# Kernel optimization log

Measured on AMD Instinct MI355X. Metric: run time of the kernel, lower is better.

Reference implementation:

```python
import jax, jax.numpy as jnp
import numpy as np

B, T, C = 8, 1024, 1024
EPS = 1e-5
NEG_INF = -1e38


def layernorm(x, w, b):
    mu = jnp.mean(x, axis=-1, keepdims=True)
    var = jnp.var(x, axis=-1, keepdims=True)
    return (x - mu) * jax.lax.rsqrt(var + EPS) * w + b


def wkv_scan(w, u, k, v):
    """Numerically-stable RWKV-4 WKV recurrence (forward direction).
    w: [C] (negative decay), u: [C] bonus, k, v: [B, T, C]. Returns [B, T, C]."""
    kt = jnp.swapaxes(k, 0, 1)  # [T, B, C]
    vt = jnp.swapaxes(v, 0, 1)
    bsz = k.shape[0]
    a0 = jnp.zeros((bsz, C), k.dtype)
    b0 = jnp.zeros((bsz, C), k.dtype)
    p0 = jnp.full((bsz, C), NEG_INF, k.dtype)

    def step(carry, inp):
        a, b, p = carry
        kk, vv = inp
        # output at current step (with bonus u on current token)
        q = jnp.maximum(p, u + kk)
        e1 = jnp.exp(p - q)
        e2 = jnp.exp(u + kk - q)
        out = (e1 * a + e2 * vv) / (e1 * b + e2)
        # decay state and absorb current token
        q2 = jnp.maximum(p + w, kk)
        f1 = jnp.exp(p + w - q2)
        f2 = jnp.exp(kk - q2)
        return (f1 * a + f2 * vv, f1 * b + f2, q2), out

    _, outs = jax.lax.scan(step, (a0, b0, p0), (kt, vt))
    return jnp.swapaxes(outs, 0, 1)  # [B, T, C]


def setup_inputs() -> dict:
    key = jax.random.key(0)
    ks = jax.random.split(key, 12)
    s = 0.02
    d = {}
    d["x"] = jax.random.normal(ks[0], (B, T, C), jnp.float32)
    d["ln1_w"] = jnp.ones((C,), jnp.float32)
    d["ln1_b"] = jnp.zeros((C,), jnp.float32)
    d["ln2_w"] = jnp.ones((C,), jnp.float32)
    d["ln2_b"] = jnp.zeros((C,), jnp.float32)
    d["Wr"] = jax.random.normal(ks[1], (C, C), jnp.float32) * s
    d["Wk"] = jax.random.normal(ks[2], (C, C), jnp.float32) * s
    d["Wv"] = jax.random.normal(ks[3], (C, C), jnp.float32) * s
    d["Wo"] = jax.random.normal(ks[4], (C, C), jnp.float32) * s
    d["decay"] = jax.random.normal(ks[5], (C,), jnp.float32) * 0.1
    d["u"] = jax.random.normal(ks[6], (C,), jnp.float32) * 0.1
    d["Wfk"] = jax.random.normal(ks[7], (4 * C, C), jnp.float32) * s
    d["Wfv"] = jax.random.normal(ks[8], (C, 4 * C), jnp.float32) * s
    d["Wfr"] = jax.random.normal(ks[9], (C, C), jnp.float32) * s
    return d


def reference(x, ln1_w, ln1_b, ln2_w, ln2_b, Wr, Wk, Wv, Wo, decay, u, Wfk, Wfv, Wfr):
    # --- bidirectional time-mix (WKV attention) ---
    xn = layernorm(x, ln1_w, ln1_b)
    r = jax.nn.sigmoid(xn @ Wr.T)
    k = xn @ Wk.T
    v = xn @ Wv.T
    w = -jnp.exp(decay)  # per-channel negative decay
    wkv_f = wkv_scan(w, u, k, v)
    wkv_b = jnp.flip(wkv_scan(w, u, jnp.flip(k, axis=1), jnp.flip(v, axis=1)), axis=1)
    wkv = 0.5 * (wkv_f + wkv_b)
    x = x + (r * wkv) @ Wo.T
    # --- channel-mix FFN ---
    xn2 = layernorm(x, ln2_w, ln2_b)
    kk = jnp.square(jax.nn.relu(xn2 @ Wfk.T))  # [B, T, 4C]
    x = x + jax.nn.sigmoid(xn2 @ Wfr.T) * (kk @ Wfv.T)
    return x
```

## Files before the change

kernel.cpp:

```cpp
#include <hip/hip_runtime.h>
#include <cstdint>
#include <cstddef>

typedef unsigned short u16;
typedef __bf16 bf16_t;
typedef bf16_t bf16x8 __attribute__((ext_vector_type(8)));
typedef float f32x4 __attribute__((ext_vector_type(4)));

#define GCH 16
#define TCH 64

static __device__ __forceinline__ float bf2f(u16 v) {
    union { unsigned int u; float f; } cv;
    cv.u = ((unsigned int)v) << 16;
    return cv.f;
}
static __device__ __forceinline__ u16 f2bf(float f) {
    union { float f; unsigned int u; } cv;
    cv.f = f;
    unsigned int r = 0x7fffu + ((cv.u >> 16) & 1u);
    return (u16)((cv.u + r) >> 16);
}

struct F2BFSegs { const float* src[7]; u16* dst[7]; int n4[7]; };

__global__ __launch_bounds__(256)
void f2bf_all(F2BFSegs s)
{
    const int seg = blockIdx.y;
    const int i = blockIdx.x * 256 + threadIdx.x;
    if (i < s.n4[seg]) {
        float4 f = ((const float4*)s.src[seg])[i];
        ushort4 o;
        o.x = f2bf(f.x); o.y = f2bf(f.y); o.z = f2bf(f.z); o.w = f2bf(f.w);
        ((ushort4*)s.dst[seg])[i] = o;
    }
}

template<int BF16IN>
__global__ __launch_bounds__(256)
void ln_kernel(const void* __restrict__ xin, const float* __restrict__ w,
               const float* __restrict__ b, u16* __restrict__ out)
{
    const int row = blockIdx.x;
    const int tid = threadIdx.x;
    float vals[4];
    if (BF16IN) {
        const ushort4 uv = ((const ushort4*)((const u16*)xin + (size_t)row * 1024))[tid];
        vals[0] = bf2f(uv.x); vals[1] = bf2f(uv.y);
        vals[2] = bf2f(uv.z); vals[3] = bf2f(uv.w);
    } else {
        const float4 f = ((const float4*)((const float*)xin + (size_t)row * 1024))[tid];
        vals[0] = f.x; vals[1] = f.y; vals[2] = f.z; vals[3] = f.w;
    }
    float s  = vals[0] + vals[1] + vals[2] + vals[3];
    float ss = vals[0]*vals[0] + vals[1]*vals[1] + vals[2]*vals[2] + vals[3]*vals[3];
    for (int off = 32; off; off >>= 1) {
        s  += __shfl_down(s, off, 64);
        ss += __shfl_down(ss, off, 64);
    }
    __shared__ float redS[4], redQ[4];
    if ((tid & 63) == 0) { redS[tid >> 6] = s; redQ[tid >> 6] = ss; }
    __syncthreads();
    s  = redS[0] + redS[1] + redS[2] + redS[3];
    ss = redQ[0] + redQ[1] + redQ[2] + redQ[3];
    const float mu  = s * (1.f / 1024.f);
    const float var = ss * (1.f / 1024.f) - mu * mu;
    const float rs  = rsqrtf(var + 1e-5f);
    const float4 wv = ((const float4*)w)[tid];
    const float4 bv = ((const float4*)b)[tid];
    ushort4 o;
    o.x = f2bf((vals[0] - mu) * rs * wv.x + bv.x);
    o.y = f2bf((vals[1] - mu) * rs * wv.y + bv.y);
    o.z = f2bf((vals[2] - mu) * rs * wv.z + bv.z);
    o.w = f2bf((vals[3] - mu) * rs * wv.w + bv.w);
    ((ushort4*)(out + (size_t)row * 1024))[tid] = o;
}

template<int EPI>
__global__ __launch_bounds__(256)
void gemm_bt(const u16* __restrict__ A, const u16* __restrict__ B,
             int M, int N, int K,
             void* __restrict__ outp,
             const void* __restrict__ aux1, const void* __restrict__ aux2)
{
    __shared__ u16 lA[128 * 64];
    __shared__ u16 lB[128 * 64];
    const int tid  = threadIdx.x;
    const int wave = tid >> 6;
    const int lane = tid & 63;
    const int q    = lane >> 4;
    const int l16  = lane & 15;
    const long mBase = (long)blockIdx.x * 128;
    const long nBase = (long)blockIdx.y * 128;
    const int wm = (wave >> 1) * 64;
    const int wn = (wave & 1) * 64;

    f32x4 acc[4][4];
#pragma unroll
    for (int i = 0; i < 4; ++i)
#pragma unroll
        for (int j = 0; j < 4; ++j)
#pragma unroll
            for (int r = 0; r < 4; ++r) acc[i][j][r] = 0.f;

    const int srow = tid >> 3;
    const int scol = ((tid & 7) ^ (srow & 7)) * 8;
    const int ldsW = wave * 512;
    const int swz = l16 & 7;

    for (int kb = 0; kb < K; kb += 64) {
        __syncthreads();
#pragma unroll
        for (int c = 0; c < 4; ++c) {
            const int row = c * 32 + srow;
            const u16* ga = A + (mBase + row) * (long)K + kb + scol;
            const u16* gb = B + (nBase + row) * (long)K + kb + scol;
            __builtin_amdgcn_global_load_lds(
                (const __attribute__((address_space(1))) void*)ga,
                (__attribute__((address_space(3))) void*)(lA + c * 2048 + ldsW),
                16, 0, 0);
            __builtin_amdgcn_global_load_lds(
                (const __attribute__((address_space(1))) void*)gb,
                (__attribute__((address_space(3))) void*)(lB + c * 2048 + ldsW),
                16, 0, 0);
        }
        __syncthreads();
#pragma unroll
        for (int ks = 0; ks < 2; ++ks) {
            const int grp = ((ks * 4 + q) ^ swz) * 8;
            bf16x8 af[4], bfm[4];
#pragma unroll
            for (int i = 0; i < 4; ++i) {
                af[i]  = *(const bf16x8*)(lA + (wm + i * 16 + l16) * 64 + grp);
                bfm[i] = *(const bf16x8*)(lB + (wn + i * 16 + l16) * 64 + grp);
            }
#pragma unroll
            for (int i = 0; i < 4; ++i)
#pragma unroll
                for (int j = 0; j < 4; ++j)
                    acc[i][j] = __builtin_amdgcn_mfma_f32_16x16x32_bf16(
                        af[i], bfm[j], acc[i][j], 0, 0, 0);
        }
    }

    if (EPI == 5 || EPI == 6) {
        u16* optr; long sN, cb;
        if (EPI == 5) {
            const long seg = nBase >> 10;
            optr = (u16*)(seg == 0 ? outp
                        : seg == 1 ? (void*)aux1 : (void*)aux2);
            sN = 1024; cb = (nBase & 1023) + wn + l16;
        } else {
            if (nBase < 4096) { optr = (u16*)outp; sN = 4096; cb = nBase + wn + l16; }
            else { optr = (u16*)aux1; sN = 1024; cb = (nBase - 4096) + wn + l16; }
        }
#pragma unroll
        for (int i = 0; i < 4; ++i)
#pragma unroll
            for (int r = 0; r < 4; ++r) {
                const long row = mBase + wm + i * 16 + q * 4 + r;
                const long rowOff = row * sN + cb;
#pragma unroll
                for (int j = 0; j < 4; ++j) {
                    const float val = acc[i][j][r];
                    float t;
                    if (EPI == 5) t = val;
                    else if (nBase < 4096) t = val > 0.f ? val * val : 0.f;
                    else t = __fdividef(1.f, 1.f + __expf(-val));
                    optr[rowOff + j * 16] = f2bf(t);
                }
            }
    } else {
        const long colBase = nBase + wn + l16;
#pragma unroll
        for (int i = 0; i < 4; ++i) {
#pragma unroll
            for (int r = 0; r < 4; ++r) {
                const long row = mBase + wm + i * 16 + q * 4 + r;
                const long rowOff = row * (long)N;
#pragma unroll
                for (int j = 0; j < 4; ++j) {
                    const long idx = rowOff + colBase + j * 16;
                    const float val = acc[i][j][r];
                    if (EPI == 1) {
                        ((u16*)outp)[idx] = f2bf(((const float*)aux1)[idx] + val);
                    } else {
                        const float t = bf2f(((const u16*)aux1)[idx])
                                      + bf2f(((const u16*)aux2)[idx]) * val;
                        ((float*)outp)[idx] = t;
                    }
                }
            }
        }
    }
}

__global__ __launch_bounds__(64)
void wkv_sum(const u16* __restrict__ kbuf, const u16* __restrict__ vbuf,
             const float* __restrict__ decay,
             float* __restrict__ sumA, float* __restrict__ sumB,
             float* __restrict__ sumP)
{
    const int c   = blockIdx.x * 64 + threadIdx.x;
    const int bt  = blockIdx.y;
    const int dir = blockIdx.z & 1;
    const int g   = blockIdx.z >> 1;
    const long base = (long)bt * (1024 * 1024) + c;
    const long stride = dir ? -1024 : 1024;
    long idx = dir ? base + (long)(1023 - g * TCH) * 1024
                   : base + (long)(g * TCH) * 1024;
    const float w = -__expf(decay[c]);
    float a = 0.f, b = 0.f, p = -1e38f;

    float kq[8], vq[8];
#pragma unroll
    for (int j = 0; j < 8; ++j) {
        kq[j] = bf2f(kbuf[idx + j * stride]);
        vq[j] = bf2f(vbuf[idx + j * stride]);
    }
    for (int tb = 0; tb < TCH / 8; ++tb) {
        float kn[8], vn[8];
        if (tb < TCH / 8 - 1) {
#pragma unroll
            for (int j = 0; j < 8; ++j) {
                kn[j] = bf2f(kbuf[idx + (j + 8) * stride]);
                vn[j] = bf2f(vbuf[idx + (j + 8) * stride]);
            }
        }
#pragma unroll
        for (int j = 0; j < 8; ++j) {
            const float kk = kq[j], vv = vq[j];
            const float pw = p + w;
            const float d  = pw - kk;
            const float e  = __expf(-fabsf(d));
            const float f1 = d >= 0.f ? 1.f : e;
            const float f2 = d >= 0.f ? e : 1.f;
            a = f1 * a + f2 * vv;
            b = f1 * b + f2;
            p = fmaxf(pw, kk);
        }
#pragma unroll
        for (int j = 0; j < 8; ++j) { kq[j] = kn[j]; vq[j] = vn[j]; }
        idx += 8 * stride;
    }
    const int sidx = (((dir * GCH + g) * 8 + bt) << 10) + c;
    sumA[sidx] = a; sumB[sidx] = b; sumP[sidx] = p;
}

__global__ __launch_bounds__(64)
void wkv_out2(const u16* __restrict__ kbuf, const u16* __restrict__ vbuf,
              const float* __restrict__ decay, const float* __restrict__ uarr,
              const float* __restrict__ sumA, const float* __restrict__ sumB,
              const float* __restrict__ sumP,
              const u16* __restrict__ rpre, u16* __restrict__ rwkv)
{
    __shared__ float fbuf[TCH * 64];
    const int lane = threadIdx.x;
    const int c   = blockIdx.x * 64 + lane;
    const int bt  = blockIdx.y;
    const int g   = blockIdx.z;
    const long base = (long)bt * (1024 * 1024) + c;
    const long rowBase = base + (long)(g * TCH) * 1024;
    const float w  = -__expf(decay[c]);
    const float uu = uarr[c];

    {
        float a = 0.f, b = 0.f, p = -1e38f;
        for (int gg = 0; gg < g; ++gg) {
            const int sidx = ((gg * 8 + bt) << 10) + c;
            const float a2 = sumA[sidx], b2 = sumB[sidx], p2 = sumP[sidx];
            const float pd = p + w * (float)TCH;
            const float d  = pd - p2;
            const float e  = __expf(-fabsf(d));
            const float x1 = d >= 0.f ? 1.f : e;
            const float x2 = d >= 0.f ? e : 1.f;
            a = x1 * a + x2 * a2;
            b = x1 * b + x2 * b2;
            p = fmaxf(pd, p2);
        }
        long idx = rowBase;
        float kq[8], vq[8];
#pragma unroll
        for (int j = 0; j < 8; ++j) {
            kq[j] = bf2f(kbuf[idx + j * 1024]);
            vq[j] = bf2f(vbuf[idx + j * 1024]);
        }
        for (int tb = 0; tb < TCH / 8; ++tb) {
            float kn[8], vn[8];
            if (tb < TCH / 8 - 1) {
#pragma unroll
                for (int j = 0; j < 8; ++j) {
                    kn[j] = bf2f(kbuf[idx + (j + 8) * 1024]);
                    vn[j] = bf2f(vbuf[idx + (j + 8) * 1024]);
                }
            }
#pragma unroll
            for (int j = 0; j < 8; ++j) {
                const float kk = kq[j], vv = vq[j];
                const float uk = uu + kk;
                const float d1 = p - uk;
                const float e  = __expf(-fabsf(d1));
                const float e1 = d1 >= 0.f ? 1.f : e;
                const float e2 = d1 >= 0.f ? e : 1.f;
                fbuf[(tb * 8 + j) * 64 + lane] =
                    __fdividef(e1 * a + e2 * vv, e1 * b + e2);
                const float pw = p + w;
                const float d2 = pw - kk;
                const float e_ = __expf(-fabsf(d2));
                const float f1 = d2 >= 0.f ? 1.f : e_;
                const float f2 = d2 >= 0.f ? e_ : 1.f;
                a = f1 * a + f2 * vv;
                b = f1 * b + f2;
                p = fmaxf(pw, kk);
            }
#pragma unroll
            for (int j = 0; j < 8; ++j) { kq[j] = kn[j]; vq[j] = vn[j]; }
            idx += 8 * 1024;
        }
    }
    __syncthreads();

    {
        float a = 0.f, b = 0.f, p = -1e38f;
        const int gb = GCH - 1 - g;
        for (int gg = 0; gg < gb; ++gg) {
            const int sidx = (((GCH + gg) * 8 + bt) << 10) + c;
            const float a2 = sumA[sidx], b2 = sumB[sidx], p2 = sumP[sidx];
            const float pd = p + w * (float)TCH;
            const float d  = pd - p2;
            const float e  = __expf(-fabsf(d));
            const float x1 = d >= 0.f ? 1.f : e;
            const float x2 = d >= 0.f ? e : 1.f;
            a = x1 * a + x2 * a2;
            b = x1 * b + x2 * b2;
            p = fmaxf(pd, p2);
        }
        long idx = rowBase + (long)(TCH - 1) * 1024;
        float kq[8], vq[8];
#pragma unroll
        for (int j = 0; j < 8; ++j) {
            kq[j] = bf2f(kbuf[idx - j * 1024]);
            vq[j] = bf2f(vbuf[idx - j * 1024]);
        }
        for (int tb = 0; tb < TCH / 8; ++tb) {
            float kn[8], vn[8];
            if (tb < TCH / 8 - 1) {
#pragma unroll
                for (int j = 0; j < 8; ++j) {
                    kn[j] = bf2f(kbuf[idx - (j + 8) * 1024]);
                    vn[j] = bf2f(vbuf[idx - (j + 8) * 1024]);
                }
            }
#pragma unroll
            for (int j = 0; j < 8; ++j) {
                const long ii = idx - (long)j * 1024;
                const int  tl = TCH - 1 - (tb * 8 + j);
                const float kk = kq[j], vv = vq[j];
                const float uk = uu + kk;
                const float d1 = p - uk;
                const float e  = __expf(-fabsf(d1));
                const float e1 = d1 >= 0.f ? 1.f : e;
                const float e2 = d1 >= 0.f ? e : 1.f;
                const float ob = __fdividef(e1 * a + e2 * vv, e1 * b + e2);
                const float of = fbuf[tl * 64 + lane];
                const float rr = __fdividef(1.f, 1.f + __expf(-bf2f(rpre[ii])));
                rwkv[ii] = f2bf(rr * 0.5f * (of + ob));
                const float pw = p + w;
                const float d2 = pw - kk;
                const float e_ = __expf(-fabsf(d2));
                const float f1 = d2 >= 0.f ? 1.f : e_;
                const float f2 = d2 >= 0.f ? e_ : 1.f;
                a = f1 * a + f2 * vv;
                b = f1 * b + f2;
                p = fmaxf(pw, kk);
            }
#pragma unroll
            for (int j = 0; j < 8; ++j) { kq[j] = kn[j]; vq[j] = vn[j]; }
            idx -= 8 * 1024;
        }
    }
}

extern "C" void kernel_launch(void* const* d_in, const int* in_sizes, int n_in,
                              void* d_out, int out_size, void* d_ws, size_t ws_size,
                              hipStream_t stream)
{
    (void)in_sizes; (void)n_in; (void)out_size; (void)ws_size;
    const float* x     = (const float*)d_in[0];
    const float* ln1w  = (const float*)d_in[1];
    const float* ln1b  = (const float*)d_in[2];
    const float* ln2w  = (const float*)d_in[3];
    const float* ln2b  = (const float*)d_in[4];
    const float* Wr    = (const float*)d_in[5];
    const float* Wk    = (const float*)d_in[6];
    const float* Wv    = (const float*)d_in[7];
    const float* Wo    = (const float*)d_in[8];
    const float* decay = (const float*)d_in[9];
    const float* uarr  = (const float*)d_in[10];
    const float* Wfk   = (const float*)d_in[11];
    const float* Wfv   = (const float*)d_in[12];
    const float* Wfr   = (const float*)d_in[13];

    const int M = 8192, C = 1024, C4 = 4096;
    const size_t MB = 1024u * 1024u;
    char* ws = (char*)d_ws;
    u16*  X2    = (u16*)(ws);
    u16*  XN    = (u16*)(ws + 16 * MB);
    u16*  RP    = (u16*)(ws + 32 * MB);
    u16*  KB    = (u16*)(ws + 48 * MB);
    u16*  VB    = (u16*)(ws + 64 * MB);
    u16*  RWKV  = (u16*)(ws + 80 * MB);
    u16*  KK    = (u16*)(ws + 48 * MB);
    float* sumA = (float*)(ws + 112 * MB);
    float* sumB = (float*)(ws + 113 * MB);
    float* sumP = (float*)(ws + 114 * MB);
    u16*  WrB   = (u16*)(ws + 116 * MB);
    u16*  WkB   = (u16*)(ws + 118 * MB);
    u16*  WvB   = (u16*)(ws + 120 * MB);
    u16*  WoB   = (u16*)(ws + 122 * MB);
    u16*  WfkB  = (u16*)(ws + 124 * MB);
    u16*  WfrB  = (u16*)(ws + 132 * MB);
    u16*  WfvB  = (u16*)(ws + 134 * MB);

    const dim3 blk(256);
    const int n4_1M = C * C / 4, n4_4M = C * C4 / 4;

    F2BFSegs segs;
    segs.src[0] = Wr;  segs.dst[0] = WrB;  segs.n4[0] = n4_1M;
    segs.src[1] = Wk;  segs.dst[1] = WkB;  segs.n4[1] = n4_1M;
    segs.src[2] = Wv;  segs.dst[2] = WvB;  segs.n4[2] = n4_1M;
    segs.src[3] = Wo;  segs.dst[3] = WoB;  segs.n4[3] = n4_1M;
    segs.src[4] = Wfk; segs.dst[4] = WfkB; segs.n4[4] = n4_4M;
    segs.src[5] = Wfr; segs.dst[5] = WfrB; segs.n4[5] = n4_1M;
    segs.src[6] = Wfv; segs.dst[6] = WfvB; segs.n4[6] = n4_4M;
    f2bf_all<<<dim3(n4_4M / 256, 7), blk, 0, stream>>>(segs);

    ln_kernel<0><<<dim3(M), blk, 0, stream>>>(x, ln1w, ln1b, XN);
    gemm_bt<5><<<dim3(M / 128, 3 * C / 128), blk, 0, stream>>>(
        XN, WrB, M, 3 * C, C, RP, KB, VB);
    wkv_sum<<<dim3(16, 8, 2 * GCH), dim3(64), 0, stream>>>(KB, VB, decay,
                                                           sumA, sumB, sumP);
    wkv_out2<<<dim3(16, 8, GCH), dim3(64), 0, stream>>>(KB, VB, decay, uarr,
                                                        sumA, sumB, sumP,
                                                        RP, RWKV);
    gemm_bt<1><<<dim3(M / 128, C / 128), blk, 0, stream>>>(
        RWKV, WoB, M, C, C, X2, x, nullptr);
    ln_kernel<1><<<dim3(M), blk, 0, stream>>>(X2, ln2w, ln2b, XN);
    gemm_bt<6><<<dim3(M / 128, 5 * C / 128), blk, 0, stream>>>(
        XN, WfkB, M, 5 * C, C, KK, RP, nullptr);
    gemm_bt<4><<<dim3(M / 128, C / 128), blk, 0, stream>>>(
        KK, WfvB, M, C, C4, d_out, X2, RP);
}
```

Before: 462.1 us.

## Run FFN key/receptance GEMM in FP8 with scaled MFMA

Converts the Wfk/Wfr weights (pre-scaled by 16) and the second layernorm output to FP8, and adds a new GEMM kernel that uses the MX-scaled 16x16x128 FP8 MFMA with direct global-to-LDS loads. The fused relu-square and sigmoid epilogue moves into this kernel. The goal is to halve operand bytes and double matrix throughput for the largest GEMM. The cost is reduced precision, which risks accuracy tolerance, especially for squared-relu outputs.

After: 411.5 us. -11.0%, faster.

```diff
diff --git a/kernel.cpp b/kernel.cpp
--- a/kernel.cpp
+++ b/kernel.cpp
@@ -3,9 +3,12 @@
 #include <cstddef>
 
 typedef unsigned short u16;
+typedef unsigned char u8;
+typedef unsigned int u32;
 typedef __bf16 bf16_t;
 typedef bf16_t bf16x8 __attribute__((ext_vector_type(8)));
 typedef float f32x4 __attribute__((ext_vector_type(4)));
+typedef int i32x8 __attribute__((ext_vector_type(8)));
 
 #define GCH 16
 #define TCH 64
@@ -22,25 +25,30 @@
     return (u16)((cv.u + r) >> 16);
 }
 
-struct F2BFSegs { const float* src[7]; u16* dst[7]; int n4[7]; };
+struct WSegs { const float* src[7]; void* dst[7]; int n4[7]; int mode[7]; };
 
 __global__ __launch_bounds__(256)
-void f2bf_all(F2BFSegs s)
+void wconv_all(WSegs s)
 {
     const int seg = blockIdx.y;
     const int i = blockIdx.x * 256 + threadIdx.x;
-    if (i < s.n4[seg]) {
-        float4 f = ((const float4*)s.src[seg])[i];
+    if (i >= s.n4[seg]) return;
+    float4 f = ((const float4*)s.src[seg])[i];
+    if (s.mode[seg] == 0) {
         ushort4 o;
         o.x = f2bf(f.x); o.y = f2bf(f.y); o.z = f2bf(f.z); o.w = f2bf(f.w);
         ((ushort4*)s.dst[seg])[i] = o;
-    }
-}
-
-template<int BF16IN>
+    } else {
+        const int p0 = __builtin_amdgcn_cvt_pk_fp8_f32(f.x * 16.f, f.y * 16.f, 0, 0);
+        const int p1 = __builtin_amdgcn_cvt_pk_fp8_f32(f.z * 16.f, f.w * 16.f, 0, 0);
+        ((u32*)s.dst[seg])[i] = (u32)(p0 & 0xFFFF) | ((u32)p1 << 16);
+    }
+}
+
+template<int BF16IN, int OUT8>
 __global__ __launch_bounds__(256)
 void ln_kernel(const void* __restrict__ xin, const float* __restrict__ w,
-               const float* __restrict__ b, u16* __restrict__ out)
+               const float* __restrict__ b, void* __restrict__ out)
 {
     const int row = blockIdx.x;
     const int tid = threadIdx.x;
@@ -69,12 +77,19 @@
     const float rs  = rsqrtf(var + 1e-5f);
     const float4 wv = ((const float4*)w)[tid];
     const float4 bv = ((const float4*)b)[tid];
-    ushort4 o;
-    o.x = f2bf((vals[0] - mu) * rs * wv.x + bv.x);
-    o.y = f2bf((vals[1] - mu) * rs * wv.y + bv.y);
-    o.z = f2bf((vals[2] - mu) * rs * wv.z + bv.z);
-    o.w = f2bf((vals[3] - mu) * rs * wv.w + bv.w);
-    ((ushort4*)(out + (size_t)row * 1024))[tid] = o;
+    const float o0 = (vals[0] - mu) * rs * wv.x + bv.x;
+    const float o1 = (vals[1] - mu) * rs * wv.y + bv.y;
+    const float o2 = (vals[2] - mu) * rs * wv.z + bv.z;
+    const float o3 = (vals[3] - mu) * rs * wv.w + bv.w;
+    if (OUT8) {
+        const int p0 = __builtin_amdgcn_cvt_pk_fp8_f32(o0, o1, 0, 0);
+        const int p1 = __builtin_amdgcn_cvt_pk_fp8_f32(o2, o3, 0, 0);
+        ((u32*)out)[(size_t)row * 256 + tid] = (u32)(p0 & 0xFFFF) | ((u32)p1 << 16);
+    } else {
+        ushort4 o;
+        o.x = f2bf(o0); o.y = f2bf(o1); o.z = f2bf(o2); o.w = f2bf(o3);
+        ((ushort4*)out)[(size_t)row * 256 + tid] = o;
+    }
 }
 
 template<int EPI>
@@ -144,32 +159,18 @@
         }
     }
 
-    if (EPI == 5 || EPI == 6) {
-        u16* optr; long sN, cb;
-        if (EPI == 5) {
-            const long seg = nBase >> 10;
-            optr = (u16*)(seg == 0 ? outp
-                        : seg == 1 ? (void*)aux1 : (void*)aux2);
-            sN = 1024; cb = (nBase & 1023) + wn + l16;
-        } else {
-            if (nBase < 4096) { optr = (u16*)outp; sN = 4096; cb = nBase + wn + l16; }
-            else { optr = (u16*)aux1; sN = 1024; cb = (nBase - 4096) + wn + l16; }
-        }
+    if (EPI == 5) {
+        const long seg = nBase >> 10;
+        u16* optr = (u16*)(seg == 0 ? outp : seg == 1 ? (void*)aux1 : (void*)aux2);
+        const long cb = (nBase & 1023) + wn + l16;
 #pragma unroll
         for (int i = 0; i < 4; ++i)
 #pragma unroll
             for (int r = 0; r < 4; ++r) {
-                const long row = mBase + wm + i * 16 + q * 4 + r;
-                const long rowOff = row * sN + cb;
-#pragma unroll
-                for (int j = 0; j < 4; ++j) {
-                    const float val = acc[i][j][r];
-                    float t;
-                    if (EPI == 5) t = val;
-                    else if (nBase < 4096) t = val > 0.f ? val * val : 0.f;
-                    else t = __fdividef(1.f, 1.f + __expf(-val));
-                    optr[rowOff + j * 16] = f2bf(t);
-                }
+                const long rowOff = (mBase + wm + i * 16 + q * 4 + r) * 1024 + cb;
+#pragma unroll
+                for (int j = 0; j < 4; ++j)
+                    optr[rowOff + j * 16] = f2bf(acc[i][j][r]);
             }
     } else {
         const long colBase = nBase + wn + l16;
@@ -194,6 +195,100 @@
             }
         }
     }
+}
+
+__global__ __launch_bounds__(256)
+void gemm_f8(const u8* __restrict__ A, const u8* __restrict__ B,
+             int M, int N, int K,
+             u16* __restrict__ kk, u16* __restrict__ rp)
+{
+    __shared__ __align__(16) u8 lA[128 * 128];
+    __shared__ __align__(16) u8 lB[128 * 128];
+    const int tid  = threadIdx.x;
+    const int wave = tid >> 6;
+    const int lane = tid & 63;
+    const int q    = lane >> 4;
+    const int l16  = lane & 15;
+    const long mBase = (long)blockIdx.x * 128;
+    const long nBase = (long)blockIdx.y * 128;
+    const int wm = (wave >> 1) * 64;
+    const int wn = (wave & 1) * 64;
+
+    f32x4 acc[4][4];
+#pragma unroll
+    for (int i = 0; i < 4; ++i)
+#pragma unroll
+        for (int j = 0; j < 4; ++j)
+#pragma unroll
+            for (int r = 0; r < 4; ++r) acc[i][j][r] = 0.f;
+
+    const int srow  = tid >> 3;
+    const int scolB = ((tid & 7) ^ (srow & 7)) * 16;
+    const int ldsW  = wave * 1024;
+    const int swz   = l16 & 7;
+
+    for (int kb = 0; kb < K; kb += 128) {
+        __syncthreads();
+#pragma unroll
+        for (int c = 0; c < 4; ++c) {
+            const int row = c * 32 + srow;
+            const u8* ga = A + (mBase + row) * (long)K + kb + scolB;
+            const u8* gb = B + (nBase + row) * (long)K + kb + scolB;
+            __builtin_amdgcn_global_load_lds(
+                (const __attribute__((address_space(1))) void*)ga,
+                (__attribute__((address_space(3))) void*)(lA + c * 4096 + ldsW),
+                16, 0, 0);
+            __builtin_amdgcn_global_load_lds(
+                (const __attribute__((address_space(1))) void*)gb,
+                (__attribute__((address_space(3))) void*)(lB + c * 4096 + ldsW),
+                16, 0, 0);
+        }
+        __syncthreads();
+        const int u0 = ((2 * q) ^ swz) * 16;
+        const int u1 = ((2 * q + 1) ^ swz) * 16;
+        i32x8 af[4], bfm[4];
+#pragma unroll
+        for (int i = 0; i < 4; ++i) {
+            {
+                const u8* base = lA + (wm + i * 16 + l16) * 128;
+                const uint4 lo = *(const uint4*)(base + u0);
+                const uint4 hi = *(const uint4*)(base + u1);
+                af[i][0] = lo.x; af[i][1] = lo.y; af[i][2] = lo.z; af[i][3] = lo.w;
+                af[i][4] = hi.x; af[i][5] = hi.y; af[i][6] = hi.z; af[i][7] = hi.w;
+            }
+            {
+                const u8* base = lB + (wn + i * 16 + l16) * 128;
+                const uint4 lo = *(const uint4*)(base + u0);
+                const uint4 hi = *(const uint4*)(base + u1);
+                bfm[i][0] = lo.x; bfm[i][1] = lo.y; bfm[i][2] = lo.z; bfm[i][3] = lo.w;
+                bfm[i][4] = hi.x; bfm[i][5] = hi.y; bfm[i][6] = hi.z; bfm[i][7] = hi.w;
+            }
+        }
+#pragma unroll
+        for (int i = 0; i < 4; ++i)
+#pragma unroll
+            for (int j = 0; j < 4; ++j)
+                acc[i][j] = __builtin_amdgcn_mfma_scale_f32_16x16x128_f8f6f4(
+                    af[i], bfm[j], acc[i][j], 0, 0, 0, 127, 0, 123);
+    }
+
+    u16* optr; long sN, cb;
+    if (nBase < 4096) { optr = kk; sN = 4096; cb = nBase + wn + l16; }
+    else              { optr = rp; sN = 1024; cb = (nBase - 4096) + wn + l16; }
+#pragma unroll
+    for (int i = 0; i < 4; ++i)
+#pragma unroll
+        for (int r = 0; r < 4; ++r) {
+            const long rowOff = (mBase + wm + i * 16 + q * 4 + r) * sN + cb;
+#pragma unroll
+            for (int j = 0; j < 4; ++j) {
+                const float val = acc[i][j][r];
+                float t;
+                if (nBase < 4096) t = val > 0.f ? val * val : 0.f;
+                else t = __fdividef(1.f, 1.f + __expf(-val));
+                optr[rowOff + j * 16] = f2bf(t);
+            }
+        }
 }
 
 __global__ __launch_bounds__(64)
@@ -407,6 +502,7 @@
     char* ws = (char*)d_ws;
     u16*  X2    = (u16*)(ws);
     u16*  XN    = (u16*)(ws + 16 * MB);
+    u8*   XN8   = (u8*)(ws + 16 * MB);
     u16*  RP    = (u16*)(ws + 32 * MB);
     u16*  KB    = (u16*)(ws + 48 * MB);
     u16*  VB    = (u16*)(ws + 64 * MB);
@@ -419,24 +515,24 @@
     u16*  WkB   = (u16*)(ws + 118 * MB);
     u16*  WvB   = (u16*)(ws + 120 * MB);
     u16*  WoB   = (u16*)(ws + 122 * MB);
-    u16*  WfkB  = (u16*)(ws + 124 * MB);
-    u16*  WfrB  = (u16*)(ws + 132 * MB);
-    u16*  WfvB  = (u16*)(ws + 134 * MB);
+    u8*   Wf8   = (u8*)(ws + 124 * MB);
+    u8*   Wfr8  = (u8*)(ws + 128 * MB);
+    u16*  WfvB  = (u16*)(ws + 130 * MB);
 
     const dim3 blk(256);
     const int n4_1M = C * C / 4, n4_4M = C * C4 / 4;
 
-    F2BFSegs segs;
-    segs.src[0] = Wr;  segs.dst[0] = WrB;  segs.n4[0] = n4_1M;
-    segs.src[1] = Wk;  segs.dst[1] = WkB;  segs.n4[1] = n4_1M;
-    segs.src[2] = Wv;  segs.dst[2] = WvB;  segs.n4[2] = n4_1M;
-    segs.src[3] = Wo;  segs.dst[3] = WoB;  segs.n4[3] = n4_1M;
-    segs.src[4] = Wfk; segs.dst[4] = WfkB; segs.n4[4] = n4_4M;
-    segs.src[5] = Wfr; segs.dst[5] = WfrB; segs.n4[5] = n4_1M;
-    segs.src[6] = Wfv; segs.dst[6] = WfvB; segs.n4[6] = n4_4M;
-    f2bf_all<<<dim3(n4_4M / 256, 7), blk, 0, stream>>>(segs);
-
-    ln_kernel<0><<<dim3(M), blk, 0, stream>>>(x, ln1w, ln1b, XN);
+    WSegs segs;
+    segs.src[0] = Wr;  segs.dst[0] = WrB;  segs.n4[0] = n4_1M; segs.mode[0] = 0;
+    segs.src[1] = Wk;  segs.dst[1] = WkB;  segs.n4[1] = n4_1M; segs.mode[1] = 0;
+    segs.src[2] = Wv;  segs.dst[2] = WvB;  segs.n4[2] = n4_1M; segs.mode[2] = 0;
+    segs.src[3] = Wo;  segs.dst[3] = WoB;  segs.n4[3] = n4_1M; segs.mode[3] = 0;
+    segs.src[4] = Wfk; segs.dst[4] = Wf8;  segs.n4[4] = n4_4M; segs.mode[4] = 1;
+    segs.src[5] = Wfr; segs.dst[5] = Wfr8; segs.n4[5] = n4_1M; segs.mode[5] = 1;
+    segs.src[6] = Wfv; segs.dst[6] = WfvB; segs.n4[6] = n4_4M; segs.mode[6] = 0;
+    wconv_all<<<dim3(n4_4M / 256, 7), blk, 0, stream>>>(segs);
+
+    ln_kernel<0, 0><<<dim3(M), blk, 0, stream>>>(x, ln1w, ln1b, XN);
     gemm_bt<5><<<dim3(M / 128, 3 * C / 128), blk, 0, stream>>>(
         XN, WrB, M, 3 * C, C, RP, KB, VB);
     wkv_sum<<<dim3(16, 8, 2 * GCH), dim3(64), 0, stream>>>(KB, VB, decay,
@@ -446,9 +542,9 @@
                                                         RP, RWKV);
     gemm_bt<1><<<dim3(M / 128, C / 128), blk, 0, stream>>>(
         RWKV, WoB, M, C, C, X2, x, nullptr);
-    ln_kernel<1><<<dim3(M), blk, 0, stream>>>(X2, ln2w, ln2b, XN);
-    gemm_bt<6><<<dim3(M / 128, 5 * C / 128), blk, 0, stream>>>(
-        XN, WfkB, M, 5 * C, C, KK, RP, nullptr);
+    ln_kernel<1, 1><<<dim3(M), blk, 0, stream>>>(X2, ln2w, ln2b, XN8);
+    gemm_f8<<<dim3(M / 128, 5 * C / 128), blk, 0, stream>>>(
+        XN8, Wf8, M, 5 * C, C, KK, RP);
     gemm_bt<4><<<dim3(M / 128, C / 128), blk, 0, stream>>>(
         KK, WfvB, M, C, C4, d_out, X2, RP);
 }
```
